# Kernel tuning notes

Hardware: AMD Instinct MI355X
Metric: run time of the kernel (lower is better)

The kernel has to match this reference:

```python
import jax, jax.numpy as jnp
import numpy as np

N, F, D, H, L = 1536, 6, 64, 4, 2
DH = D // H
FF = 4 * D
EPS = 1e-5

def setup_inputs() -> dict:
    key = jax.random.key(0)
    ks = iter(jax.random.split(key, 32))
    def g(shape, scale=0.05):
        return jax.random.normal(next(ks), shape, jnp.float32) * scale
    return dict(
        node_feats=g((N, F), 1.0),
        proj_w=g((D, F)), proj_b=g((D,)),
        in_w=g((L, 3 * D, D)), in_b=g((L, 3 * D)),
        out_w=g((L, D, D)), out_b=g((L, D)),
        ff1_w=g((L, FF, D)), ff1_b=g((L, FF)),
        ff2_w=g((L, D, FF)), ff2_b=g((L, D)),
        ln1_g=jnp.ones((L, D), jnp.float32), ln1_b=jnp.zeros((L, D), jnp.float32),
        ln2_g=jnp.ones((L, D), jnp.float32), ln2_b=jnp.zeros((L, D), jnp.float32),
        ns_w=g((1, D)), ns_b=g((1,)),
        e1_w=g((D, 2 * D)), e1_b=g((D,)),
        e2_w=g((1, D)), e2_b=g((1,)),
    )

def _layernorm(x, g, b):
    mu = x.mean(-1, keepdims=True)
    var = ((x - mu) ** 2).mean(-1, keepdims=True)
    return (x - mu) / jnp.sqrt(var + EPS) * g + b

def _forward(node_feats, proj_w, proj_b, in_w, in_b, out_w, out_b,
             ff1_w, ff1_b, ff2_w, ff2_b, ln1_g, ln1_b, ln2_g, ln2_b,
             ns_w, ns_b, e1_w, e1_b, e2_w, e2_b):
    x = node_feats @ proj_w.T + proj_b  # (N, D)
    # Transformer encoder, post-norm, eval mode (dropout off); seq_len=N, batch=1.
    for l in range(L):
        qkv = x @ in_w[l].T + in_b[l]  # (N, 3D)
        q, k, v = jnp.split(qkv, 3, axis=-1)
        q = q.reshape(N, H, DH).transpose(1, 0, 2)  # (H, N, DH)
        k = k.reshape(N, H, DH).transpose(1, 0, 2)
        v = v.reshape(N, H, DH).transpose(1, 0, 2)
        scores = jnp.einsum('hnd,hmd->hnm', q, k) / jnp.sqrt(jnp.float32(DH))
        attn = jax.nn.softmax(scores, axis=-1)
        o = jnp.einsum('hnm,hmd->hnd', attn, v).transpose(1, 0, 2).reshape(N, D)
        sa = o @ out_w[l].T + out_b[l]
        x = _layernorm(x + sa, ln1_g[l], ln1_b[l])
        ff = jax.nn.relu(x @ ff1_w[l].T + ff1_b[l]) @ ff2_w[l].T + ff2_b[l]
        x = _layernorm(x + ff, ln2_g[l], ln2_b[l])
    node_logits = (x @ ns_w.T + ns_b)[:, 0]  # (N,)
    # Edge scoring: Linear(2D->D) on concat[x_i, x_j] == x_i @ A^T + x_j @ B^T + b1.
    # Precompute the two projections to avoid materializing the (N, N, 2D) concat.
    A, B = e1_w[:, :D], e1_w[:, D:]
    u = x @ A.T  # (N, D)
    w = x @ B.T  # (N, D)
    h = jax.nn.relu(u[:, None, :] + w[None, :, :] + e1_b)  # (N, N, D)
    edge_logits = jnp.einsum('nmd,d->nm', h, e2_w[0]) + e2_b[0]
    return node_logits, edge_logits

def reference(node_feats, proj_w, proj_b, in_w, in_b, out_w, out_b,
              ff1_w, ff1_b, ff2_w, ff2_b, ln1_g, ln1_b, ln2_g, ln2_b,
              ns_w, ns_b, e1_w, e1_b, e2_w, e2_b):
    return _forward(node_feats, proj_w, proj_b, in_w, in_b, out_w, out_b,
                    ff1_w, ff1_b, ff2_w, ff2_b, ln1_g, ln1_b, ln2_g, ln2_b,
                    ns_w, ns_b, e1_w, e1_b, e2_w, e2_b)
```

## Files before the change

kernel.cpp:

```cpp
#include <hip/hip_runtime.h>
#include <hip/hip_bf16.h>

#define N 1536
#define F 6
#define D 64
#define H 4
#define DH 16
#define FFDIM 256
#define NL 2
#define EPS 1e-5f
#define KS 8
#define KB (N / KS)
#define KW (KB / 4)
#define QB 128
#define NPART KS

static __device__ __forceinline__ float dot4(float4 a, float4 b) {
    return a.x * b.x + a.y * b.y + a.z * b.z + a.w * b.w;
}

__global__ __launch_bounds__(192) void k_qkv0(const float* __restrict__ nf,
                                              const float* __restrict__ pw,
                                              const float* __restrict__ pb,
                                              const float* __restrict__ w,
                                              const float* __restrict__ b,
                                              float* __restrict__ x,
                                              float* __restrict__ qkv) {
    __shared__ __align__(16) float sx[8][D];
    int n0 = blockIdx.x * 8;
    int t = threadIdx.x;
    for (int i = t; i < 8 * D; i += 192) {
        int r = i >> 6, d = i & 63;
        float acc = pb[d];
#pragma unroll
        for (int f = 0; f < F; ++f) acc += nf[(n0 + r) * F + f] * pw[d * F + f];
        sx[r][d] = acc;
        x[(n0 + r) * D + d] = acc;
    }
    __syncthreads();
    const float4* wr = (const float4*)(w + t * D);
    float acc[8];
    float bb = b[t];
#pragma unroll
    for (int r = 0; r < 8; ++r) acc[r] = bb;
#pragma unroll
    for (int e = 0; e < D / 4; ++e) {
        float4 wv = wr[e];
#pragma unroll
        for (int r = 0; r < 8; ++r) acc[r] += dot4(wv, *(const float4*)&sx[r][e * 4]);
    }
#pragma unroll
    for (int r = 0; r < 8; ++r) qkv[(n0 + r) * (3 * D) + t] = acc[r];
}

__global__ __launch_bounds__(192) void k_qkv(const float* __restrict__ x,
                                             const float* __restrict__ w,
                                             const float* __restrict__ b,
                                             float* __restrict__ qkv) {
    __shared__ __align__(16) float sx[8][D];
    int n0 = blockIdx.x * 8;
    int t = threadIdx.x;
    if (t < 128) {
        int r = t >> 4, c4 = (t & 15) * 4;
        *(float4*)&sx[r][c4] = *(const float4*)&x[(n0 + r) * D + c4];
    }
    __syncthreads();
    const float4* wr = (const float4*)(w + t * D);
    float acc[8];
    float bb = b[t];
#pragma unroll
    for (int r = 0; r < 8; ++r) acc[r] = bb;
#pragma unroll
    for (int e = 0; e < D / 4; ++e) {
        float4 wv = wr[e];
#pragma unroll
        for (int r = 0; r < 8; ++r) acc[r] += dot4(wv, *(const float4*)&sx[r][e * 4]);
    }
#pragma unroll
    for (int r = 0; r < 8; ++r) qkv[(n0 + r) * (3 * D) + t] = acc[r];
}

struct SmemKV { float k[KB][DH]; float v[KB][DH]; };
__global__ __launch_bounds__(256) void k_attn_part(const float* __restrict__ qkv,
                                                   float* __restrict__ accp,
                                                   float* __restrict__ psump) {
    __shared__ __align__(16) union {
        SmemKV kv;
        float rd[4][QB][DH + 1];
    } sm;
    int ks = blockIdx.x, qc = blockIdx.y, h = blockIdx.z;
    int t = threadIdx.x;
    int wv = t >> 6, lane = t & 63;

    for (int i = t; i < KB * 4; i += 256) {
        int row = i >> 2, c4 = (i & 3) * 4;
        const float* base = qkv + (size_t)(ks * KB + row) * (3 * D) + D + h * DH + c4;
        *(float4*)&sm.kv.k[row][c4] = *(const float4*)base;
        *(float4*)&sm.kv.v[row][c4] = *(const float4*)(base + D);
    }

    float q[2][DH];
#pragma unroll
    for (int j = 0; j < 2; ++j) {
        const float4* qp =
            (const float4*)(qkv + (size_t)(qc * QB + j * 64 + lane) * (3 * D) + h * DH);
#pragma unroll
        for (int e = 0; e < 4; ++e) {
            float4 v = qp[e];
            q[j][e * 4 + 0] = v.x * 0.25f;
            q[j][e * 4 + 1] = v.y * 0.25f;
            q[j][e * 4 + 2] = v.z * 0.25f;
            q[j][e * 4 + 3] = v.w * 0.25f;
        }
    }
    __syncthreads();

    float acc[2][DH];
#pragma unroll
    for (int j = 0; j < 2; ++j)
#pragma unroll
        for (int i = 0; i < DH; ++i) acc[j][i] = 0.f;
    float psum[2] = {0.f, 0.f};

#pragma unroll 2
    for (int jk = 0; jk < KW; ++jk) {
        int r = wv * KW + jk;
        float4 k0 = *(const float4*)&sm.kv.k[r][0];
        float4 k1 = *(const float4*)&sm.kv.k[r][4];
        float4 k2 = *(const float4*)&sm.kv.k[r][8];
        float4 k3 = *(const float4*)&sm.kv.k[r][12];
        float p[2];
#pragma unroll
        for (int j = 0; j < 2; ++j) {
            float s = q[j][0] * k0.x + q[j][1] * k0.y + q[j][2] * k0.z + q[j][3] * k0.w
                    + q[j][4] * k1.x + q[j][5] * k1.y + q[j][6] * k1.z + q[j][7] * k1.w
                    + q[j][8] * k2.x + q[j][9] * k2.y + q[j][10] * k2.z + q[j][11] * k2.w
                    + q[j][12] * k3.x + q[j][13] * k3.y + q[j][14] * k3.z + q[j][15] * k3.w;
            p[j] = __expf(s);
            psum[j] += p[j];
        }
        float4 v0 = *(const float4*)&sm.kv.v[r][0];
        float4 v1 = *(const float4*)&sm.kv.v[r][4];
        float4 v2 = *(const float4*)&sm.kv.v[r][8];
        float4 v3 = *(const float4*)&sm.kv.v[r][12];
#pragma unroll
        for (int j = 0; j < 2; ++j) {
            acc[j][0] += p[j] * v0.x;  acc[j][1] += p[j] * v0.y;
            acc[j][2] += p[j] * v0.z;  acc[j][3] += p[j] * v0.w;
            acc[j][4] += p[j] * v1.x;  acc[j][5] += p[j] * v1.y;
            acc[j][6] += p[j] * v1.z;  acc[j][7] += p[j] * v1.w;
            acc[j][8] += p[j] * v2.x;  acc[j][9] += p[j] * v2.y;
            acc[j][10] += p[j] * v2.z; acc[j][11] += p[j] * v2.w;
            acc[j][12] += p[j] * v3.x; acc[j][13] += p[j] * v3.y;
            acc[j][14] += p[j] * v3.z; acc[j][15] += p[j] * v3.w;
        }
    }

    __syncthreads();
#pragma unroll
    for (int j = 0; j < 2; ++j) {
        int qq = j * 64 + lane;
#pragma unroll
        for (int i = 0; i < DH; ++i) sm.rd[wv][qq][i] = acc[j][i];
        sm.rd[wv][qq][DH] = psum[j];
    }
    __syncthreads();

    for (int i = t; i < QB * (DH + 1); i += 256) {
        int qq = i / (DH + 1), c = i % (DH + 1);
        float s = sm.rd[0][qq][c] + sm.rd[1][qq][c] + sm.rd[2][qq][c] + sm.rd[3][qq][c];
        int n = qc * QB + qq;
        if (c < DH)
            accp[((size_t)ks * N + n) * D + h * DH + c] = s;
        else
            psump[((size_t)ks * N + n) * H + h] = s;
    }
}

__global__ __launch_bounds__(256) void k_attn_ffn(const float* __restrict__ accp,
                                                  const float* __restrict__ psump,
                                                  const float* __restrict__ ow,
                                                  const float* __restrict__ ob,
                                                  const float* __restrict__ g1,
                                                  const float* __restrict__ be1,
                                                  const float* __restrict__ w1,
                                                  const float* __restrict__ b1,
                                                  const float* __restrict__ w2,
                                                  const float* __restrict__ b2,
                                                  const float* __restrict__ g2,
                                                  const float* __restrict__ be2,
                                                  float* __restrict__ x,
                                                  int tail,
                                                  const float* __restrict__ nsw,
                                                  const float* __restrict__ nsb,
                                                  const float* __restrict__ e1w,
                                                  const float* __restrict__ e1b,
                                                  float* __restrict__ nodeo,
                                                  float* __restrict__ u,
                                                  float* __restrict__ wbuf) {
    __shared__ __align__(16) float so[4][D];
    __shared__ __align__(16) float sx[4][D];
    __shared__ __align__(16) float sh[4][FFDIM];
    __shared__ float sp[4][4][D];
    int t = threadIdx.x;
    int r = t >> 6, e = t & 63;
    int n = blockIdx.x * 4 + r;

    {
        float a = 0.f, p = 0.f;
#pragma unroll
        for (int pp = 0; pp < NPART; ++pp) {
            a += accp[((size_t)pp * N + n) * D + e];
            p += psump[((size_t)pp * N + n) * H + (e >> 4)];
        }
        so[r][e] = a / p;
    }
    __syncthreads();

    {
        const float4* ir = (const float4*)so[r];
        const float4* wr = (const float4*)(ow + e * D);
        float acc = ob[e];
#pragma unroll
        for (int k = 0; k < D / 4; ++k) acc += dot4(ir[k], wr[k]);
        float y = x[n * D + e] + acc;
        float mu = y;
#pragma unroll
        for (int off = 32; off; off >>= 1) mu += __shfl_xor(mu, off, 64);
        mu *= (1.f / 64.f);
        float diff = y - mu;
        float var = diff * diff;
#pragma unroll
        for (int off = 32; off; off >>= 1) var += __shfl_xor(var, off, 64);
        var *= (1.f / 64.f);
        sx[r][e] = diff * rsqrtf(var + EPS) * g1[e] + be1[e];
    }
    __syncthreads();

    {
        const float4* wr = (const float4*)(w1 + t * D);
        float acc[4];
        float bb = b1[t];
#pragma unroll
        for (int rr = 0; rr < 4; ++rr) acc[rr] = bb;
#pragma unroll
        for (int k = 0; k < D / 4; ++k) {
            float4 wv = wr[k];
#pragma unroll
            for (int rr = 0; rr < 4; ++rr) acc[rr] += dot4(wv, *(const float4*)&sx[rr][k * 4]);
        }
#pragma unroll
        for (int rr = 0; rr < 4; ++rr) sh[rr][t] = fmaxf(acc[rr], 0.f);
    }
    __syncthreads();

    {
        int d = t & 63, c = t >> 6;
        const float4* wr = (const float4*)(w2 + d * FFDIM + c * 64);
        float acc[4] = {0.f, 0.f, 0.f, 0.f};
#pragma unroll
        for (int k = 0; k < 16; ++k) {
            float4 wv = wr[k];
#pragma unroll
            for (int rr = 0; rr < 4; ++rr)
                acc[rr] += dot4(wv, *(const float4*)&sh[rr][c * 64 + k * 4]);
        }
#pragma unroll
        for (int rr = 0; rr < 4; ++rr) sp[rr][c][d] = acc[rr];
    }
    __syncthreads();

    {
        float y = sx[r][e] + b2[e] + sp[r][0][e] + sp[r][1][e] + sp[r][2][e] + sp[r][3][e];
        float mu = y;
#pragma unroll
        for (int off = 32; off; off >>= 1) mu += __shfl_xor(mu, off, 64);
        mu *= (1.f / 64.f);
        float diff = y - mu;
        float var = diff * diff;
#pragma unroll
        for (int off = 32; off; off >>= 1) var += __shfl_xor(var, off, 64);
        var *= (1.f / 64.f);
        float xv = diff * rsqrtf(var + EPS) * g2[e] + be2[e];
        x[n * D + e] = xv;
        sx[r][e] = xv;
    }

    if (!tail) return;
    __syncthreads();

    {
        const float4* xr = (const float4*)sx[r];
        const float4* ar = (const float4*)(e1w + e * 2 * D);
        const float4* br = (const float4*)(e1w + e * 2 * D + D);
        float au = 0.f, aw = 0.f;
#pragma unroll
        for (int k = 0; k < D / 4; ++k) {
            float4 xv = xr[k], av = ar[k], bv = br[k];
            au += dot4(xv, av);
            aw += dot4(xv, bv);
        }
        u[n * D + e] = au + e1b[e];
        wbuf[n * D + e] = aw;
        float p = sx[r][e] * nsw[e];
#pragma unroll
        for (int off = 32; off; off >>= 1) p += __shfl_xor(p, off, 64);
        if (e == 0) nodeo[n] = p + nsb[0];
    }
}

__global__ __launch_bounds__(256) void k_edge(const float* __restrict__ u,
                                              const float* __restrict__ w,
                                              const float* __restrict__ e2w,
                                              const float* __restrict__ e2b,
                                              float* __restrict__ out) {
    __shared__ __align__(16) float su[64][68];
    __shared__ __align__(16) float sw[64][68];
    __shared__ __align__(16) float sv[64];
    int tn = blockIdx.y * 64, tm = blockIdx.x * 64;
    int t = threadIdx.x;
    for (int i = t; i < 64 * 16; i += 256) {
        int r = i >> 4, c4 = (i & 15) * 4;
        *(float4*)&su[r][c4] = *(const float4*)&u[(tn + r) * D + c4];
        *(float4*)&sw[r][c4] = *(const float4*)&w[(tm + r) * D + c4];
    }
    if (t < 64) sv[t] = e2w[t];
    __syncthreads();
    float eb = e2b[0];
    int c0 = t & 15, r0 = t >> 4;

    float acc[4][4];
#pragma unroll
    for (int j = 0; j < 4; ++j)
#pragma unroll
        for (int k = 0; k < 4; ++k) acc[j][k] = 0.f;

#pragma unroll 4
    for (int e0 = 0; e0 < 64; e0 += 4) {
        float4 vv = *(const float4*)&sv[e0];
        float4 a[4], bb[4];
#pragma unroll
        for (int j = 0; j < 4; ++j) a[j] = *(const float4*)&su[r0 + 16 * j][e0];
#pragma unroll
        for (int k = 0; k < 4; ++k) bb[k] = *(const float4*)&sw[c0 + 16 * k][e0];
#pragma unroll
        for (int j = 0; j < 4; ++j)
#pragma unroll
            for (int k = 0; k < 4; ++k) {
                acc[j][k] += fmaxf(a[j].x + bb[k].x, 0.f) * vv.x;
                acc[j][k] += fmaxf(a[j].y + bb[k].y, 0.f) * vv.y;
                acc[j][k] += fmaxf(a[j].z + bb[k].z, 0.f) * vv.z;
                acc[j][k] += fmaxf(a[j].w + bb[k].w, 0.f) * vv.w;
            }
    }
#pragma unroll
    for (int j = 0; j < 4; ++j)
#pragma unroll
        for (int k = 0; k < 4; ++k)
            out[(size_t)(tn + r0 + 16 * j) * N + (tm + c0 + 16 * k)] = acc[j][k] + eb;
}

extern "C" void kernel_launch(void* const* d_in, const int* in_sizes, int n_in,
                              void* d_out, int out_size, void* d_ws, size_t ws_size,
                              hipStream_t stream) {
    const float* node_feats = (const float*)d_in[0];
    const float* proj_w = (const float*)d_in[1];
    const float* proj_b = (const float*)d_in[2];
    const float* in_w = (const float*)d_in[3];
    const float* in_b = (const float*)d_in[4];
    const float* out_w = (const float*)d_in[5];
    const float* out_b = (const float*)d_in[6];
    const float* ff1_w = (const float*)d_in[7];
    const float* ff1_b = (const float*)d_in[8];
    const float* ff2_w = (const float*)d_in[9];
    const float* ff2_b = (const float*)d_in[10];
    const float* ln1_g = (const float*)d_in[11];
    const float* ln1_b = (const float*)d_in[12];
    const float* ln2_g = (const float*)d_in[13];
    const float* ln2_b = (const float*)d_in[14];
    const float* ns_w = (const float*)d_in[15];
    const float* ns_b = (const float*)d_in[16];
    const float* e1_w = (const float*)d_in[17];
    const float* e1_b = (const float*)d_in[18];
    const float* e2_w = (const float*)d_in[19];
    const float* e2_b = (const float*)d_in[20];

    float* out = (float*)d_out;

    float* x = (float*)d_ws;
    float* qkv = x + N * D;
    float* accp = qkv + N * 3 * D;
    float* psump = accp + (size_t)NPART * N * D;
    float* u = psump + (size_t)NPART * N * H;
    float* wbuf = u + N * D;

    for (int l = 0; l < NL; ++l) {
        if (l == 0)
            k_qkv0<<<N / 8, 192, 0, stream>>>(node_feats, proj_w, proj_b,
                                              in_w, in_b, x, qkv);
        else
            k_qkv<<<N / 8, 192, 0, stream>>>(
                x, in_w + (size_t)l * 3 * D * D, in_b + (size_t)l * 3 * D, qkv);
        {
            dim3 grid(KS, N / QB, H);
            k_attn_part<<<grid, 256, 0, stream>>>(qkv, accp, psump);
        }
        k_attn_ffn<<<N / 4, 256, 0, stream>>>(
            accp, psump, out_w + (size_t)l * D * D, out_b + (size_t)l * D,
            ln1_g + (size_t)l * D, ln1_b + (size_t)l * D,
            ff1_w + (size_t)l * FFDIM * D, ff1_b + (size_t)l * FFDIM,
            ff2_w + (size_t)l * D * FFDIM, ff2_b + (size_t)l * D,
            ln2_g + (size_t)l * D, ln2_b + (size_t)l * D, x,
            (l == NL - 1) ? 1 : 0, ns_w, ns_b, e1_w, e1_b, out, u, wbuf);
    }

    {
        dim3 grid(N / 64, N / 64);
        k_edge<<<grid, 256, 0, stream>>>(u, wbuf, e2_w, e2_b, out + N);
    }
}
```

Measured before the change: 116.6 us.

## Fuse input projection and layer-0 QKV into attention; fold layer-1 QKV into FFN

Layer 0 now gets its own attention kernel. It folds the 6-to-64 input projection into the QKV weights, giving an effective 48x6 matrix per head, and computes K, V and Q straight from node features. This removes the separate qkv kernels. The layer-1 QKV projection is appended to the end of the layer-0 FFN kernel. Together this cuts the launch count from 7 to 5 and drops the qkv round trip for layer 0. The cost is redundant recomputation of the effective weights and K/V in every attention block, plus a different floating-point summation order.

```diff
diff --git a/kernel.cpp b/kernel.cpp
--- a/kernel.cpp
+++ b/kernel.cpp
@@ -19,65 +19,157 @@
     return a.x * b.x + a.y * b.y + a.z * b.z + a.w * b.w;
 }
 
-__global__ __launch_bounds__(192) void k_qkv0(const float* __restrict__ nf,
-                                              const float* __restrict__ pw,
-                                              const float* __restrict__ pb,
-                                              const float* __restrict__ w,
-                                              const float* __restrict__ b,
-                                              float* __restrict__ x,
-                                              float* __restrict__ qkv) {
-    __shared__ __align__(16) float sx[8][D];
-    int n0 = blockIdx.x * 8;
+union SmA {
+    float sinw[48][D];
+    struct { float k[KB][DH]; float v[KB][DH]; } kv;
+    float rd[4][QB][DH + 1];
+};
+__global__ __launch_bounds__(256) void k_attn0(const float* __restrict__ nf,
+                                               const float* __restrict__ pw,
+                                               const float* __restrict__ pb,
+                                               const float* __restrict__ iw,
+                                               const float* __restrict__ ib,
+                                               float* __restrict__ x,
+                                               float* __restrict__ accp,
+                                               float* __restrict__ psump) {
+    __shared__ __align__(16) SmA sm;
+    __shared__ float pwl[D * F];
+    __shared__ float pbl[D];
+    __shared__ float nfk[KB * F];
+    __shared__ float nfq[QB * F];
+    __shared__ float eff[48][F];
+    __shared__ float beff[48];
+    int ks = blockIdx.x, qc = blockIdx.y, h = blockIdx.z;
     int t = threadIdx.x;
-    for (int i = t; i < 8 * D; i += 192) {
-        int r = i >> 6, d = i & 63;
-        float acc = pb[d];
-#pragma unroll
-        for (int f = 0; f < F; ++f) acc += nf[(n0 + r) * F + f] * pw[d * F + f];
-        sx[r][d] = acc;
-        x[(n0 + r) * D + d] = acc;
-    }
-    __syncthreads();
-    const float4* wr = (const float4*)(w + t * D);
-    float acc[8];
-    float bb = b[t];
-#pragma unroll
-    for (int r = 0; r < 8; ++r) acc[r] = bb;
-#pragma unroll
-    for (int e = 0; e < D / 4; ++e) {
-        float4 wv = wr[e];
-#pragma unroll
-        for (int r = 0; r < 8; ++r) acc[r] += dot4(wv, *(const float4*)&sx[r][e * 4]);
-    }
-#pragma unroll
-    for (int r = 0; r < 8; ++r) qkv[(n0 + r) * (3 * D) + t] = acc[r];
-}
-
-__global__ __launch_bounds__(192) void k_qkv(const float* __restrict__ x,
-                                             const float* __restrict__ w,
-                                             const float* __restrict__ b,
-                                             float* __restrict__ qkv) {
-    __shared__ __align__(16) float sx[8][D];
-    int n0 = blockIdx.x * 8;
-    int t = threadIdx.x;
-    if (t < 128) {
-        int r = t >> 4, c4 = (t & 15) * 4;
-        *(float4*)&sx[r][c4] = *(const float4*)&x[(n0 + r) * D + c4];
-    }
-    __syncthreads();
-    const float4* wr = (const float4*)(w + t * D);
-    float acc[8];
-    float bb = b[t];
-#pragma unroll
-    for (int r = 0; r < 8; ++r) acc[r] = bb;
-#pragma unroll
-    for (int e = 0; e < D / 4; ++e) {
-        float4 wv = wr[e];
-#pragma unroll
-        for (int r = 0; r < 8; ++r) acc[r] += dot4(wv, *(const float4*)&sx[r][e * 4]);
-    }
-#pragma unroll
-    for (int r = 0; r < 8; ++r) qkv[(n0 + r) * (3 * D) + t] = acc[r];
+    int wv = t >> 6, lane = t & 63;
+
+    for (int i = t; i < D * F; i += 256) pwl[i] = pw[i];
+    if (t < D) pbl[t] = pb[t];
+    for (int i = t; i < KB * F; i += 256) nfk[i] = nf[ks * KB * F + i];
+    for (int i = t; i < QB * F; i += 256) nfq[i] = nf[qc * QB * F + i];
+    for (int i = t; i < 48 * D; i += 256) {
+        int oo = i >> 6, e = i & 63;
+        int o = (oo < 16) ? (h * DH + oo)
+              : (oo < 32) ? (D + h * DH + (oo - 16))
+                          : (2 * D + h * DH + (oo - 32));
+        sm.sinw[oo][e] = iw[o * D + e];
+    }
+    __syncthreads();
+
+    for (int i = t; i < 48 * F; i += 256) {
+        int oo = i / F, fx = i % F;
+        float a = 0.f;
+#pragma unroll 8
+        for (int e = 0; e < D; ++e) a += sm.sinw[oo][e] * pwl[e * F + fx];
+        eff[oo][fx] = a;
+    }
+    for (int i = t; i < 48; i += 256) {
+        int o = (i < 16) ? (h * DH + i)
+              : (i < 32) ? (D + h * DH + (i - 16))
+                         : (2 * D + h * DH + (i - 32));
+        float a = ib[o];
+#pragma unroll 8
+        for (int e = 0; e < D; ++e) a += sm.sinw[i][e] * pbl[e];
+        beff[i] = a;
+    }
+    __syncthreads();
+
+    {
+        int i = t & 31, rg = t >> 5;
+        int oo = (i < 16) ? (16 + i) : (32 + (i - 16));
+        float w0 = eff[oo][0], w1 = eff[oo][1], w2 = eff[oo][2];
+        float w3 = eff[oo][3], w4 = eff[oo][4], w5 = eff[oo][5];
+        float bo = beff[oo];
+        for (int r = rg * (KB / 8); r < (rg + 1) * (KB / 8); ++r) {
+            const float* nr = &nfk[r * F];
+            float val = bo + nr[0] * w0 + nr[1] * w1 + nr[2] * w2
+                           + nr[3] * w3 + nr[4] * w4 + nr[5] * w5;
+            if (i < 16) sm.kv.k[r][i] = val;
+            else        sm.kv.v[r][i - 16] = val;
+        }
+    }
+    float q[2][DH];
+#pragma unroll
+    for (int j = 0; j < 2; ++j) {
+        const float* nr = &nfq[(j * 64 + lane) * F];
+        float n0 = nr[0], n1 = nr[1], n2 = nr[2], n3 = nr[3], n4 = nr[4], n5 = nr[5];
+#pragma unroll
+        for (int i = 0; i < DH; ++i)
+            q[j][i] = 0.25f * (beff[i] + n0 * eff[i][0] + n1 * eff[i][1] + n2 * eff[i][2]
+                                       + n3 * eff[i][3] + n4 * eff[i][4] + n5 * eff[i][5]);
+    }
+    if (ks == 0 && h == 0) {
+        for (int i = t; i < QB * D; i += 256) {
+            int row = i >> 6, e = i & 63;
+            const float* nr = &nfq[row * F];
+            float a = pbl[e];
+#pragma unroll
+            for (int f = 0; f < F; ++f) a += nr[f] * pwl[e * F + f];
+            x[(qc * QB + row) * D + e] = a;
+        }
+    }
+    __syncthreads();
+
+    float acc[2][DH];
+#pragma unroll
+    for (int j = 0; j < 2; ++j)
+#pragma unroll
+        for (int i = 0; i < DH; ++i) acc[j][i] = 0.f;
+    float psum[2] = {0.f, 0.f};
+
+#pragma unroll 2
+    for (int jk = 0; jk < KW; ++jk) {
+        int r = wv * KW + jk;
+        float4 k0 = *(const float4*)&sm.kv.k[r][0];
+        float4 k1 = *(const float4*)&sm.kv.k[r][4];
+        float4 k2 = *(const float4*)&sm.kv.k[r][8];
+        float4 k3 = *(const float4*)&sm.kv.k[r][12];
+        float p[2];
+#pragma unroll
+        for (int j = 0; j < 2; ++j) {
+            float s = q[j][0] * k0.x + q[j][1] * k0.y + q[j][2] * k0.z + q[j][3] * k0.w
+                    + q[j][4] * k1.x + q[j][5] * k1.y + q[j][6] * k1.z + q[j][7] * k1.w
+                    + q[j][8] * k2.x + q[j][9] * k2.y + q[j][10] * k2.z + q[j][11] * k2.w
+                    + q[j][12] * k3.x + q[j][13] * k3.y + q[j][14] * k3.z + q[j][15] * k3.w;
+            p[j] = __expf(s);
+            psum[j] += p[j];
+        }
+        float4 v0 = *(const float4*)&sm.kv.v[r][0];
+        float4 v1 = *(const float4*)&sm.kv.v[r][4];
+        float4 v2 = *(const float4*)&sm.kv.v[r][8];
+        float4 v3 = *(const float4*)&sm.kv.v[r][12];
+#pragma unroll
+        for (int j = 0; j < 2; ++j) {
+            acc[j][0] += p[j] * v0.x;  acc[j][1] += p[j] * v0.y;
+            acc[j][2] += p[j] * v0.z;  acc[j][3] += p[j] * v0.w;
+            acc[j][4] += p[j] * v1.x;  acc[j][5] += p[j] * v1.y;
+            acc[j][6] += p[j] * v1.z;  acc[j][7] += p[j] * v1.w;
+            acc[j][8] += p[j] * v2.x;  acc[j][9] += p[j] * v2.y;
+            acc[j][10] += p[j] * v2.z; acc[j][11] += p[j] * v2.w;
+            acc[j][12] += p[j] * v3.x; acc[j][13] += p[j] * v3.y;
+            acc[j][14] += p[j] * v3.z; acc[j][15] += p[j] * v3.w;
+        }
+    }
+
+    __syncthreads();
+#pragma unroll
+    for (int j = 0; j < 2; ++j) {
+        int qq = j * 64 + lane;
+#pragma unroll
+        for (int i = 0; i < DH; ++i) sm.rd[wv][qq][i] = acc[j][i];
+        sm.rd[wv][qq][DH] = psum[j];
+    }
+    __syncthreads();
+
+    for (int i = t; i < QB * (DH + 1); i += 256) {
+        int qq = i / (DH + 1), c = i % (DH + 1);
+        float s = sm.rd[0][qq][c] + sm.rd[1][qq][c] + sm.rd[2][qq][c] + sm.rd[3][qq][c];
+        int n = qc * QB + qq;
+        if (c < DH)
+            accp[((size_t)ks * N + n) * D + h * DH + c] = s;
+        else
+            psump[((size_t)ks * N + n) * H + h] = s;
+    }
 }
 
 struct SmemKV { float k[KB][DH]; float v[KB][DH]; };
@@ -190,6 +282,9 @@
                                                   const float* __restrict__ g2,
                                                   const float* __restrict__ be2,
                                                   float* __restrict__ x,
+                                                  const float* __restrict__ nw,
+                                                  const float* __restrict__ nb,
+                                                  float* __restrict__ nqkv,
                                                   int tail,
                                                   const float* __restrict__ nsw,
                                                   const float* __restrict__ nsb,
@@ -284,6 +379,28 @@
         float xv = diff * rsqrtf(var + EPS) * g2[e] + be2[e];
         x[n * D + e] = xv;
         sx[r][e] = xv;
+    }
+
+    if (nqkv) {
+        __syncthreads();
+        if (t < 3 * D) {
+            const float4* wr = (const float4*)(nw + t * D);
+            float bb = nb[t];
+            float a0 = bb, a1 = bb, a2 = bb, a3 = bb;
+#pragma unroll
+            for (int k = 0; k < D / 4; ++k) {
+                float4 wv = wr[k];
+                a0 += dot4(wv, *(const float4*)&sx[0][k * 4]);
+                a1 += dot4(wv, *(const float4*)&sx[1][k * 4]);
+                a2 += dot4(wv, *(const float4*)&sx[2][k * 4]);
+                a3 += dot4(wv, *(const float4*)&sx[3][k * 4]);
+            }
+            int n0 = blockIdx.x * 4;
+            nqkv[(n0 + 0) * (3 * D) + t] = a0;
+            nqkv[(n0 + 1) * (3 * D) + t] = a1;
+            nqkv[(n0 + 2) * (3 * D) + t] = a2;
+            nqkv[(n0 + 3) * (3 * D) + t] = a3;
+        }
     }
 
     if (!tail) return;
@@ -394,26 +511,24 @@
     float* u = psump + (size_t)NPART * N * H;
     float* wbuf = u + N * D;
 
-    for (int l = 0; l < NL; ++l) {
-        if (l == 0)
-            k_qkv0<<<N / 8, 192, 0, stream>>>(node_feats, proj_w, proj_b,
-                                              in_w, in_b, x, qkv);
-        else
-            k_qkv<<<N / 8, 192, 0, stream>>>(
-                x, in_w + (size_t)l * 3 * D * D, in_b + (size_t)l * 3 * D, qkv);
-        {
-            dim3 grid(KS, N / QB, H);
-            k_attn_part<<<grid, 256, 0, stream>>>(qkv, accp, psump);
-        }
-        k_attn_ffn<<<N / 4, 256, 0, stream>>>(
-            accp, psump, out_w + (size_t)l * D * D, out_b + (size_t)l * D,
-            ln1_g + (size_t)l * D, ln1_b + (size_t)l * D,
-            ff1_w + (size_t)l * FFDIM * D, ff1_b + (size_t)l * FFDIM,
-            ff2_w + (size_t)l * D * FFDIM, ff2_b + (size_t)l * D,
-            ln2_g + (size_t)l * D, ln2_b + (size_t)l * D, x,
-            (l == NL - 1) ? 1 : 0, ns_w, ns_b, e1_w, e1_b, out, u, wbuf);
-    }
-
+    dim3 agrid(KS, N / QB, H);
+
+    k_attn0<<<agrid, 256, 0, stream>>>(node_feats, proj_w, proj_b,
+                                       in_w, in_b, x, accp, psump);
+    k_attn_ffn<<<N / 4, 256, 0, stream>>>(
+        accp, psump, out_w, out_b, ln1_g, ln1_b,
+        ff1_w, ff1_b, ff2_w, ff2_b, ln2_g, ln2_b, x,
+        in_w + (size_t)3 * D * D, in_b + 3 * D, qkv,
+        0, nullptr, nullptr, nullptr, nullptr, nullptr, nullptr, nullptr);
+    k_attn_part<<<agrid, 256, 0, stream>>>(qkv, accp, psump);
+    k_attn_ffn<<<N / 4, 256, 0, stream>>>(
+        accp, psump, out_w + (size_t)D * D, out_b + D,
+        ln1_g + D, ln1_b + D,
+        ff1_w + (size_t)FFDIM * D, ff1_b + FFDIM,
+        ff2_w + (size_t)D * FFDIM, ff2_b + D,
+        ln2_g + D, ln2_b + D, x,
+        nullptr, nullptr, nullptr,
+        1, ns_w, ns_b, e1_w, e1_b, out, u, wbuf);
     {
         dim3 grid(N / 64, N / 64);
         k_edge<<<grid, 256, 0, stream>>>(u, wbuf, e2_w, e2_b, out + N);
```

After: 108.6 us. 1.07x faster.
